# Optimization experiments

Measured on AMD Instinct MI355X. Metric: run time of the kernel, lower is better.

## Reference

```python
import jax, jax.numpy as jnp
import numpy as np

B, N, FIN, HID, HEADS, LAYERS = 2048, 62, 128, 512, 8, 3
FOUT = HID // HEADS  # 64


def setup_inputs() -> dict:
    key = jax.random.key(0)
    ks = jax.random.split(key, 12)
    x = jax.random.normal(ks[0], (B, N, FIN), dtype=jnp.float32)
    adj = jax.random.randint(ks[1], (B, N, N), 0, 2, dtype=jnp.int32)
    # BatchNorm1d(62) params (eval mode, running stats)
    bn_gamma = jax.random.normal(ks[2], (N,), dtype=jnp.float32) * 0.1 + 1.0
    bn_beta = jax.random.normal(ks[3], (N,), dtype=jnp.float32) * 0.1
    bn_mean = jax.random.normal(ks[4], (N,), dtype=jnp.float32) * 0.1
    bn_var = jax.random.uniform(ks[5], (N,), dtype=jnp.float32, minval=0.5, maxval=1.5)
    # input MLP
    W_mlp = jax.random.normal(ks[6], (FIN, HID), dtype=jnp.float32) / np.sqrt(FIN)
    b_mlp = jnp.zeros((HID,), dtype=jnp.float32)
    # GAT params: one W [HID, FOUT] and one a [2*FOUT] per (layer, head)
    W_gat = jax.random.normal(ks[7], (LAYERS, HEADS, HID, FOUT), dtype=jnp.float32) / np.sqrt(HID)
    a_gat = jax.random.normal(ks[8], (LAYERS, HEADS, 2 * FOUT), dtype=jnp.float32) / np.sqrt(2 * FOUT)
    # output head
    W_out = jax.random.normal(ks[9], (HID, 3), dtype=jnp.float32) / np.sqrt(HID)
    b_out = jnp.zeros((3,), dtype=jnp.float32)
    return {
        "x": x, "adj": adj,
        "bn_gamma": bn_gamma, "bn_beta": bn_beta, "bn_mean": bn_mean, "bn_var": bn_var,
        "W_mlp": W_mlp, "b_mlp": b_mlp,
        "W_gat": W_gat, "a_gat": a_gat,
        "W_out": W_out, "b_out": b_out,
    }


def reference(x, adj, bn_gamma, bn_beta, bn_mean, bn_var, W_mlp, b_mlp, W_gat, a_gat, W_out, b_out):
    eps = 1e-5
    alpha = 0.2  # LeakyReLU slope
    # BatchNorm1d over the node dim (C=62), eval mode
    xb = (x - bn_mean[None, :, None]) * (bn_gamma / jnp.sqrt(bn_var + eps))[None, :, None] + bn_beta[None, :, None]
    h_x = xb @ W_mlp + b_mlp  # [B, N, HID]
    mask = adj > 0  # [B, N, N]
    n_layers, n_heads, _, f_out = W_gat.shape
    for l in range(n_layers):
        # all heads at once: h [H, B, N, FOUT]
        h = jnp.einsum('bnf,hfd->hbnd', h_x, W_gat[l])
        a1 = a_gat[l][:, :f_out]   # multiplies the repeat(1,N,1) part -> h_j
        a2 = a_gat[l][:, f_out:]   # multiplies the repeat(1,1,N) part -> h_i
        f1 = jnp.einsum('hbnd,hd->hbn', h, a1)  # per-node source term
        f2 = jnp.einsum('hbnd,hd->hbn', h, a2)  # per-node dest term
        # e[h,b,i,j] = leaky(a2.h_i + a1.h_j)  (matches cat/repeat layout)
        e = jax.nn.leaky_relu(f2[:, :, :, None] + f1[:, :, None, :], alpha)
        e = jnp.where(mask[None], e, jnp.float32(-9e15))
        # torch F.softmax(attention, dim=1) on [B,N,N] -> axis=2 here (the i axis)
        att = jax.nn.softmax(e, axis=2)
        hp = jnp.einsum('hbij,hbjd->hbid', att, h)
        hp = jax.nn.elu(hp)
        # concat heads on feature dim -> [B, N, HID]
        h_x = jnp.transpose(hp, (1, 2, 0, 3)).reshape(h_x.shape[0], h_x.shape[1], n_heads * f_out)
    pooled = jnp.sum(h_x, axis=1)  # [B, HID]
    logits = pooled @ W_out + b_out  # [B, 3]
    return jax.nn.log_softmax(logits, axis=-1)
```

## Files before the change

kernel.cpp:

```cpp
#include <hip/hip_runtime.h>
#include <cstdint>
#include <cstddef>

#define B_ 2048
#define N_ 62
#define FIN_ 128
#define HID_ 512
#define HEADS_ 8
#define FOUT_ 64
#define LAYERS_ 3
#define M_ (B_*N_)

typedef __bf16 bf16x8 __attribute__((ext_vector_type(8)));
typedef float  f32x4  __attribute__((ext_vector_type(4)));
typedef unsigned short u16;

static __device__ __forceinline__ u16 f2bf(float f) {
    union { float f; uint32_t u; } v; v.f = f;
    uint32_t u = v.u;
    return (u16)((u + 0x7fffu + ((u >> 16) & 1u)) >> 16);
}
static __device__ __forceinline__ float bf2f(u16 s) {
    union { uint32_t u; float f; } v; v.u = ((uint32_t)s) << 16;
    return v.f;
}
static __device__ __forceinline__ float rdlane(float v, int l) {
    union { float f; int i; } a, b; a.f = v;
    b.i = __builtin_amdgcn_readlane(a.i, l);
    return b.f;
}

__global__ __launch_bounds__(256) void repack_w(
    const float* __restrict__ Wm, const float* __restrict__ Wg,
    u16* __restrict__ wmlp_t, u16* __restrict__ wgat_t)
{
    int idx = blockIdx.x * 256 + threadIdx.x;
    const int T1 = HID_ * FIN_;
    const int T2 = LAYERS_ * HID_ * HID_;
    if (idx < T1) {
        int n = idx / FIN_, k = idx % FIN_;
        wmlp_t[idx] = f2bf(Wm[k * HID_ + n]);
    } else if (idx < T1 + T2) {
        int j = idx - T1;
        int l = j / (HID_ * HID_);
        int r = j % (HID_ * HID_);
        int n = r / HID_, k = r % HID_;
        wgat_t[j] = f2bf(Wg[(((size_t)(l * HEADS_ + (n >> 6))) * HID_ + k) * FOUT_ + (n & 63)]);
    }
}

__global__ __launch_bounds__(256) void build_masks(
    const int* __restrict__ adj, uint64_t* __restrict__ masks,
    uint64_t* __restrict__ masksT)
{
    __shared__ uint32_t m32[128];
    const int b = blockIdx.x, tid = threadIdx.x;
    if (tid < 128) m32[tid] = 0;
    __syncthreads();
    const int* a = adj + (size_t)b * N_ * N_;
    for (int idx = tid; idx < N_ * N_; idx += 256) {
        int i = idx / N_, j = idx % N_;
        if (a[idx] > 0) atomicOr(&m32[i * 2 + (j >> 5)], 1u << (j & 31));
    }
    __syncthreads();
    if (tid < 128) ((uint32_t*)(masks + (size_t)b * 64))[tid] = m32[tid];
    if (tid < 64) {
        int j = tid;
        uint64_t c = 0;
        for (int i = 0; i < N_; i++) {
            uint64_t bit = (m32[i * 2 + (j >> 5)] >> (j & 31)) & 1u;
            c |= bit << i;
        }
        masksT[(size_t)b * 64 + j] = c;
    }
}

#define S_IN 520
#define S_T  72
#define S_X  136
#define X0   28160

__global__ __launch_bounds__(512, 4) void gat_fused(
    const float* __restrict__ x,
    const float* __restrict__ bng, const float* __restrict__ bnb,
    const float* __restrict__ bnm, const float* __restrict__ bnv,
    const u16* __restrict__ wmlp_t, const float* __restrict__ bm,
    const u16* __restrict__ wgat_t, const float* __restrict__ ag,
    const uint64_t* __restrict__ masks, const uint64_t* __restrict__ masksT,
    const float* __restrict__ Wout, const float* __restrict__ bout,
    float* __restrict__ out)
{
    __shared__ __align__(16) u16 buf[36864];
    __shared__ uint64_t msk[64];
    __shared__ __align__(16) float fstat[1032];
    float* F1 = fstat;
    float* LS = fstat + 512;

    const int tid = threadIdx.x, b = blockIdx.x;
    const int wave = tid >> 6, lane = tid & 63;
    const int lr = lane & 15, lq = lane >> 4;
    const int w64 = wave * 64;

    const uint64_t cm = masksT[(size_t)b * 64 + lane];
    const uint32_t cml = (uint32_t)cm, cmh = (uint32_t)(cm >> 32);

    {
        const float* xg = x + (size_t)b * N_ * FIN_;
        for (int idx = tid; idx < 2048; idx += 512) {
            int n = idx >> 5, kq = idx & 31;
            ushort4 o = {0, 0, 0, 0};
            if (n < N_) {
                float s = bng[n] * rsqrtf(bnv[n] + 1e-5f);
                float sh = bnb[n] - bnm[n] * s;
                float4 v = *(const float4*)(xg + n * FIN_ + kq * 4);
                o.x = f2bf(v.x * s + sh); o.y = f2bf(v.y * s + sh);
                o.z = f2bf(v.z * s + sh); o.w = f2bf(v.w * s + sh);
            }
            *(ushort4*)&buf[X0 + n * S_X + kq * 4] = o;
        }
        if (tid < 64) msk[tid] = (tid < N_) ? masks[(size_t)b * 64 + tid] : 0ull;
    }
    __syncthreads();

    {
        f32x4 acc[4][4];
#pragma unroll
        for (int mt = 0; mt < 4; mt++)
#pragma unroll
            for (int nt = 0; nt < 4; nt++) acc[mt][nt] = (f32x4){0.f, 0.f, 0.f, 0.f};
        const int c0 = w64;
#pragma unroll
        for (int kt = 0; kt < 4; kt++) {
            int k0 = kt * 32;
            bf16x8 af[4];
#pragma unroll
            for (int mt = 0; mt < 4; mt++)
                af[mt] = *(const bf16x8*)&buf[X0 + (mt * 16 + lr) * S_X + k0 + lq * 8];
#pragma unroll
            for (int nt = 0; nt < 4; nt++) {
                bf16x8 bfr = *(const bf16x8*)(wmlp_t + (size_t)(c0 + nt * 16 + lr) * FIN_ + k0 + lq * 8);
#pragma unroll
                for (int mt = 0; mt < 4; mt++)
                    acc[mt][nt] = __builtin_amdgcn_mfma_f32_16x16x32_bf16(
                        af[mt], bfr, acc[mt][nt], 0, 0, 0);
            }
        }
        __syncthreads();
        float bl[4];
#pragma unroll
        for (int nt = 0; nt < 4; nt++) bl[nt] = bm[c0 + nt * 16 + lr];
#pragma unroll
        for (int mt = 0; mt < 4; mt++)
#pragma unroll
            for (int nt = 0; nt < 4; nt++)
#pragma unroll
                for (int r = 0; r < 4; r++) {
                    int row = mt * 16 + lq * 4 + r;
                    buf[row * S_IN + c0 + nt * 16 + lr] =
                        (row < N_) ? f2bf(acc[mt][nt][r] + bl[nt]) : (u16)0;
                }
    }
    __syncthreads();

#pragma unroll 1
    for (int l = 0; l < LAYERS_; l++) {
        const u16* wp = wgat_t + ((size_t)l * HID_ + w64) * HID_;
        const float* a1 = ag + (size_t)l * HEADS_ * 2 * FOUT_ + wave * 128;

        f32x4 acc[4][4];
#pragma unroll
        for (int mt = 0; mt < 4; mt++)
#pragma unroll
            for (int nt = 0; nt < 4; nt++) acc[mt][nt] = (f32x4){0.f, 0.f, 0.f, 0.f};
#pragma unroll 4
        for (int kt = 0; kt < 16; kt++) {
            int k0 = kt * 32;
            bf16x8 af[4];
#pragma unroll
            for (int mt = 0; mt < 4; mt++)
                af[mt] = *(const bf16x8*)&buf[(mt * 16 + lr) * S_IN + k0 + lq * 8];
#pragma unroll
            for (int nt = 0; nt < 4; nt++) {
                bf16x8 bfr = *(const bf16x8*)(wp + (size_t)(nt * 16 + lr) * HID_ + k0 + lq * 8);
#pragma unroll
                for (int mt = 0; mt < 4; mt++)
                    acc[mt][nt] = __builtin_amdgcn_mfma_f32_16x16x32_bf16(
                        af[mt], bfr, acc[mt][nt], 0, 0, 0);
            }
        }
        __syncthreads();

#pragma unroll
        for (int mt = 0; mt < 4; mt++)
#pragma unroll
            for (int nt = 0; nt < 4; nt++) {
                ushort4 pk;
                pk.x = f2bf(acc[mt][nt][0]); pk.y = f2bf(acc[mt][nt][1]);
                pk.z = f2bf(acc[mt][nt][2]); pk.w = f2bf(acc[mt][nt][3]);
                *(ushort4*)&buf[(w64 + nt * 16 + lr) * S_T + mt * 16 + lq * 4] = pk;
            }

        float p1 = 0.f, p2 = 0.f;
#pragma unroll 8
        for (int d = 0; d < 64; d++) {
            float hv = bf2f(buf[(w64 + d) * S_T + lane]);
            p1 = fmaf(hv, a1[d], p1);
            p2 = fmaf(hv, a1[64 + d], p2);
        }

        float M = -3.0e38f;
#pragma unroll
        for (int i = 0; i < N_; i++) {
            float f2i = rdlane(p2, i);
            uint32_t bit = ((i < 32 ? cml : cmh) >> (i & 31)) & 1u;
            M = fmaxf(M, bit ? f2i : -3.0e38f);
        }
        float vm = M + p1;
        float m = fmaxf(fmaxf(vm, 0.2f * vm), -9e15f);
        float ssum = 0.f;
#pragma unroll
        for (int i = 0; i < N_; i++) {
            float f2i = rdlane(p2, i);
            float v = f2i + p1;
            v = fmaxf(v, 0.2f * v);
            uint32_t bit = ((i < 32 ? cml : cmh) >> (i & 31)) & 1u;
            float e = bit ? v : -9e15f;
            ssum += __expf(e - m);
        }
        F1[w64 + lane] = p1;
        LS[w64 + lane] = m + __logf(ssum);

        f32x4 acc2[4][4];
#pragma unroll
        for (int mt = 0; mt < 4; mt++)
#pragma unroll
            for (int nt = 0; nt < 4; nt++) acc2[mt][nt] = (f32x4){0.f, 0.f, 0.f, 0.f};
        float f2r[4];
#pragma unroll
        for (int mt = 0; mt < 4; mt++) f2r[mt] = __shfl(p2, mt * 16 + lr, 64);
#pragma unroll
        for (int kt = 0; kt < 2; kt++) {
            int j0 = kt * 32 + lq * 8;
            f32x4 f1a = *(const f32x4*)&F1[w64 + j0];
            f32x4 f1b = *(const f32x4*)&F1[w64 + j0 + 4];
            f32x4 la  = *(const f32x4*)&LS[w64 + j0];
            f32x4 lb  = *(const f32x4*)&LS[w64 + j0 + 4];
            bf16x8 hb[4];
#pragma unroll
            for (int nt = 0; nt < 4; nt++)
                hb[nt] = *(const bf16x8*)&buf[(w64 + nt * 16 + lr) * S_T + kt * 32 + lq * 8];
#pragma unroll
            for (int mt = 0; mt < 4; mt++) {
                uint64_t mi = msk[mt * 16 + lr];
                uint32_t sh = (uint32_t)(mi >> (kt * 32)) >> (lq * 8);
                bf16x8 pf;
#pragma unroll
                for (int t = 0; t < 8; t++) {
                    float f1t = t < 4 ? f1a[t] : f1b[t - 4];
                    float lst = t < 4 ? la[t]  : lb[t - 4];
                    float v = f2r[mt] + f1t;
                    v = fmaxf(v, 0.2f * v);
                    float e = ((sh >> t) & 1u) ? v : -9e15f;
                    pf[t] = (__bf16)__expf(e - lst);
                }
#pragma unroll
                for (int nt = 0; nt < 4; nt++)
                    acc2[mt][nt] = __builtin_amdgcn_mfma_f32_16x16x32_bf16(
                        pf, hb[nt], acc2[mt][nt], 0, 0, 0);
            }
        }
        __syncthreads();

#pragma unroll
        for (int mt = 0; mt < 4; mt++)
#pragma unroll
            for (int nt = 0; nt < 4; nt++)
#pragma unroll
                for (int r = 0; r < 4; r++) {
                    float v = acc2[mt][nt][r];
                    v = v > 0.f ? v : __expf(v) - 1.f;
                    int row = mt * 16 + lq * 4 + r;
                    buf[row * S_IN + w64 + nt * 16 + lr] =
                        (row < N_) ? f2bf(v) : (u16)0;
                }
        __syncthreads();
    }

    {
        float s = 0.f;
#pragma unroll 2
        for (int n = 0; n < N_; n++) s += bf2f(buf[n * S_IN + tid]);
        fstat[tid] = s;
    }
    __syncthreads();
    if (tid < 192) {
        int c = tid >> 6, ln = tid & 63;
        float p = 0.f;
#pragma unroll
        for (int k = ln; k < HID_; k += 64) p += fstat[k] * Wout[k * 3 + c];
        for (int off = 32; off > 0; off >>= 1) p += __shfl_down(p, off, 64);
        if (ln == 0) fstat[1024 + c] = p + bout[c];
    }
    __syncthreads();
    if (tid == 0) {
        float l0 = fstat[1024], l1 = fstat[1025], l2 = fstat[1026];
        float mm = fmaxf(l0, fmaxf(l1, l2));
        float s = __expf(l0 - mm) + __expf(l1 - mm) + __expf(l2 - mm);
        float ls = mm + logf(s);
        out[b * 3 + 0] = l0 - ls;
        out[b * 3 + 1] = l1 - ls;
        out[b * 3 + 2] = l2 - ls;
    }
}

extern "C" void kernel_launch(void* const* d_in, const int* in_sizes, int n_in,
                              void* d_out, int out_size, void* d_ws, size_t ws_size,
                              hipStream_t stream)
{
    const float* x   = (const float*)d_in[0];
    const int*   adj = (const int*)d_in[1];
    const float* bng = (const float*)d_in[2];
    const float* bnb = (const float*)d_in[3];
    const float* bnm = (const float*)d_in[4];
    const float* bnv = (const float*)d_in[5];
    const float* Wm  = (const float*)d_in[6];
    const float* bm  = (const float*)d_in[7];
    const float* Wg  = (const float*)d_in[8];
    const float* ag  = (const float*)d_in[9];
    const float* Wo  = (const float*)d_in[10];
    const float* bo  = (const float*)d_in[11];
    float* out = (float*)d_out;

    uint64_t* masks  = (uint64_t*)d_ws;
    uint64_t* masksT = masks + (size_t)B_ * 64;
    u16* wmlp_t = (u16*)(masksT + (size_t)B_ * 64);
    u16* wgat_t = wmlp_t + (size_t)HID_ * FIN_;

    int rep_total = HID_ * FIN_ + LAYERS_ * HID_ * HID_;
    repack_w<<<(rep_total + 255) / 256, 256, 0, stream>>>(Wm, Wg, wmlp_t, wgat_t);
    build_masks<<<B_, 256, 0, stream>>>(adj, masks, masksT);

    gat_fused<<<B_, 512, 0, stream>>>(
        x, bng, bnb, bnm, bnv, wmlp_t, bm, wgat_t, ag,
        masks, masksT, Wo, bo, out);
}
```

Baseline: 698.8 us.

## Fold attention vectors into GAT weights and simplify softmax statistics

Precomputes W·a1 and W·a2 (scaled by log2e) as two extra output columns of each head's weight matrix, so the attention logits come out of the projection MFMA instead of a separate 64-step dot-product loop. The softmax max now uses an unmasked upper bound via a wave reduction instead of a masked 62-step scan, and exponentials use exp2. The MLP and aggregation MFMAs are transposed so results are written as packed 4-element stores. In exchange, each head does a fifth N-tile of MFMA work (80 columns, 16 of them padding), the logits are rounded to bf16 weights, and the unmasked max can underflow sums, which is guarded by a clamp.

Result: slower. 996.5 us (+42.6%).

```diff
diff --git a/kernel.cpp b/kernel.cpp
--- a/kernel.cpp
+++ b/kernel.cpp
@@ -15,6 +15,19 @@
 typedef float  f32x4  __attribute__((ext_vector_type(4)));
 typedef unsigned short u16;
 
+#define LOG2E 1.4426950408889634f
+
+#if __has_builtin(__builtin_amdgcn_exp2f)
+#define EXP2F(x) __builtin_amdgcn_exp2f(x)
+#else
+#define EXP2F(x) exp2f(x)
+#endif
+#if __has_builtin(__builtin_amdgcn_logf)
+#define LOG2F(x) __builtin_amdgcn_logf(x)
+#else
+#define LOG2F(x) log2f(x)
+#endif
+
 static __device__ __forceinline__ u16 f2bf(float f) {
     union { float f; uint32_t u; } v; v.f = f;
     uint32_t u = v.u;
@@ -32,20 +45,33 @@
 
 __global__ __launch_bounds__(256) void repack_w(
     const float* __restrict__ Wm, const float* __restrict__ Wg,
-    u16* __restrict__ wmlp_t, u16* __restrict__ wgat_t)
+    const float* __restrict__ ag,
+    u16* __restrict__ wmlp_t, u16* __restrict__ wgat2)
 {
     int idx = blockIdx.x * 256 + threadIdx.x;
     const int T1 = HID_ * FIN_;
-    const int T2 = LAYERS_ * HID_ * HID_;
+    const int T2 = LAYERS_ * HEADS_ * 80 * HID_;
     if (idx < T1) {
         int n = idx / FIN_, k = idx % FIN_;
         wmlp_t[idx] = f2bf(Wm[k * HID_ + n]);
     } else if (idx < T1 + T2) {
         int j = idx - T1;
-        int l = j / (HID_ * HID_);
-        int r = j % (HID_ * HID_);
+        int lh = j / (80 * HID_);
+        int r  = j % (80 * HID_);
         int n = r / HID_, k = r % HID_;
-        wgat_t[j] = f2bf(Wg[(((size_t)(l * HEADS_ + (n >> 6))) * HID_ + k) * FOUT_ + (n & 63)]);
+        float v;
+        if (n < 64) {
+            v = Wg[((size_t)lh * HID_ + k) * FOUT_ + n];
+        } else if (n < 66) {
+            const float* ap = ag + (size_t)lh * 128 + (n - 64) * 64;
+            const float* wrow = Wg + ((size_t)lh * HID_ + k) * FOUT_;
+            float s = 0.f;
+            for (int d = 0; d < 64; d++) s += wrow[d] * ap[d];
+            v = s * LOG2E;
+        } else {
+            v = 0.f;
+        }
+        wgat2[j] = f2bf(v);
     }
 }
 
@@ -85,16 +111,17 @@
     const float* __restrict__ bng, const float* __restrict__ bnb,
     const float* __restrict__ bnm, const float* __restrict__ bnv,
     const u16* __restrict__ wmlp_t, const float* __restrict__ bm,
-    const u16* __restrict__ wgat_t, const float* __restrict__ ag,
+    const u16* __restrict__ wgat2,
     const uint64_t* __restrict__ masks, const uint64_t* __restrict__ masksT,
     const float* __restrict__ Wout, const float* __restrict__ bout,
     float* __restrict__ out)
 {
     __shared__ __align__(16) u16 buf[36864];
     __shared__ uint64_t msk[64];
-    __shared__ __align__(16) float fstat[1032];
+    __shared__ __align__(16) float fstat[1544];
     float* F1 = fstat;
-    float* LS = fstat + 512;
+    float* F2 = fstat + 512;
+    float* LS = fstat + 1024;
 
     const int tid = threadIdx.x, b = blockIdx.x;
     const int wave = tid >> 6, lane = tid & 63;
@@ -122,6 +149,10 @@
     }
     __syncthreads();
 
+    uint64_t mi4[4];
+#pragma unroll
+    for (int it = 0; it < 4; it++) mi4[it] = msk[it * 16 + lr];
+
     {
         f32x4 acc[4][4];
 #pragma unroll
@@ -132,46 +163,54 @@
 #pragma unroll
         for (int kt = 0; kt < 4; kt++) {
             int k0 = kt * 32;
-            bf16x8 af[4];
-#pragma unroll
-            for (int mt = 0; mt < 4; mt++)
-                af[mt] = *(const bf16x8*)&buf[X0 + (mt * 16 + lr) * S_X + k0 + lq * 8];
+            bf16x8 wf[4], xf[4];
+#pragma unroll
+            for (int mt = 0; mt < 4; mt++)
+                wf[mt] = *(const bf16x8*)(wmlp_t + (size_t)(c0 + mt * 16 + lr) * FIN_ + k0 + lq * 8);
+#pragma unroll
+            for (int nt = 0; nt < 4; nt++)
+                xf[nt] = *(const bf16x8*)&buf[X0 + (nt * 16 + lr) * S_X + k0 + lq * 8];
+#pragma unroll
+            for (int mt = 0; mt < 4; mt++)
+#pragma unroll
+                for (int nt = 0; nt < 4; nt++)
+                    acc[mt][nt] = __builtin_amdgcn_mfma_f32_16x16x32_bf16(
+                        wf[mt], xf[nt], acc[mt][nt], 0, 0, 0);
+        }
+        __syncthreads();
+        f32x4 bl[4];
+#pragma unroll
+        for (int mt = 0; mt < 4; mt++)
+            bl[mt] = *(const f32x4*)&bm[c0 + mt * 16 + lq * 4];
+#pragma unroll
+        for (int mt = 0; mt < 4; mt++)
 #pragma unroll
             for (int nt = 0; nt < 4; nt++) {
-                bf16x8 bfr = *(const bf16x8*)(wmlp_t + (size_t)(c0 + nt * 16 + lr) * FIN_ + k0 + lq * 8);
-#pragma unroll
-                for (int mt = 0; mt < 4; mt++)
-                    acc[mt][nt] = __builtin_amdgcn_mfma_f32_16x16x32_bf16(
-                        af[mt], bfr, acc[mt][nt], 0, 0, 0);
-            }
-        }
-        __syncthreads();
-        float bl[4];
-#pragma unroll
-        for (int nt = 0; nt < 4; nt++) bl[nt] = bm[c0 + nt * 16 + lr];
-#pragma unroll
-        for (int mt = 0; mt < 4; mt++)
-#pragma unroll
-            for (int nt = 0; nt < 4; nt++)
-#pragma unroll
-                for (int r = 0; r < 4; r++) {
-                    int row = mt * 16 + lq * 4 + r;
-                    buf[row * S_IN + c0 + nt * 16 + lr] =
-                        (row < N_) ? f2bf(acc[mt][nt][r] + bl[nt]) : (u16)0;
-                }
+                int node = nt * 16 + lr;
+                ushort4 pk;
+                pk.x = f2bf(acc[mt][nt][0] + bl[mt][0]);
+                pk.y = f2bf(acc[mt][nt][1] + bl[mt][1]);
+                pk.z = f2bf(acc[mt][nt][2] + bl[mt][2]);
+                pk.w = f2bf(acc[mt][nt][3] + bl[mt][3]);
+                if (node < N_)
+                    *(ushort4*)&buf[node * S_IN + c0 + mt * 16 + lq * 4] = pk;
+            }
+        if (lane < 16) {
+            uint4 z = {0u, 0u, 0u, 0u};
+            *(uint4*)&buf[(N_ + (lane >> 3)) * S_IN + c0 + (lane & 7) * 8] = z;
+        }
     }
     __syncthreads();
 
 #pragma unroll 1
     for (int l = 0; l < LAYERS_; l++) {
-        const u16* wp = wgat_t + ((size_t)l * HID_ + w64) * HID_;
-        const float* a1 = ag + (size_t)l * HEADS_ * 2 * FOUT_ + wave * 128;
-
-        f32x4 acc[4][4];
-#pragma unroll
-        for (int mt = 0; mt < 4; mt++)
-#pragma unroll
-            for (int nt = 0; nt < 4; nt++) acc[mt][nt] = (f32x4){0.f, 0.f, 0.f, 0.f};
+        const u16* wp = wgat2 + (size_t)(l * HEADS_ + wave) * 80 * HID_;
+
+        f32x4 acc[4][5];
+#pragma unroll
+        for (int mt = 0; mt < 4; mt++)
+#pragma unroll
+            for (int nt = 0; nt < 5; nt++) acc[mt][nt] = (f32x4){0.f, 0.f, 0.f, 0.f};
 #pragma unroll 4
         for (int kt = 0; kt < 16; kt++) {
             int k0 = kt * 32;
@@ -180,7 +219,7 @@
             for (int mt = 0; mt < 4; mt++)
                 af[mt] = *(const bf16x8*)&buf[(mt * 16 + lr) * S_IN + k0 + lq * 8];
 #pragma unroll
-            for (int nt = 0; nt < 4; nt++) {
+            for (int nt = 0; nt < 5; nt++) {
                 bf16x8 bfr = *(const bf16x8*)(wp + (size_t)(nt * 16 + lr) * HID_ + k0 + lq * 8);
 #pragma unroll
                 for (int mt = 0; mt < 4; mt++)
@@ -188,6 +227,36 @@
                         af[mt], bfr, acc[mt][nt], 0, 0, 0);
             }
         }
+
+        if (lr < 2) {
+            float* Fp = lr ? F2 : F1;
+#pragma unroll
+            for (int mt = 0; mt < 4; mt++)
+#pragma unroll
+                for (int r = 0; r < 4; r++)
+                    Fp[w64 + mt * 16 + lq * 4 + r] = acc[mt][4][r];
+        }
+        float p1 = F1[w64 + lane];
+        float p2 = F2[w64 + lane];
+        float pm = (lane < N_) ? p2 : -3.0e38f;
+#pragma unroll
+        for (int off = 32; off; off >>= 1) pm = fmaxf(pm, __shfl_xor(pm, off, 64));
+        float vm = pm + p1;
+        float m = fmaxf(vm, 0.2f * vm);
+        float s0 = 0.f, s1 = 0.f;
+#pragma unroll
+        for (int i = 0; i < N_; i += 2) {
+            float fa = rdlane(p2, i), fb = rdlane(p2, i + 1);
+            float va = fa + p1, vb = fb + p1;
+            va = fmaxf(va, 0.2f * va); vb = fmaxf(vb, 0.2f * vb);
+            float ea = EXP2F(va - m), eb = EXP2F(vb - m);
+            uint32_t w = (i < 32) ? cml : cmh;
+            s0 += ((w >> (i & 31)) & 1u) ? ea : 0.f;
+            s1 += ((w >> ((i + 1) & 31)) & 1u) ? eb : 0.f;
+        }
+        float ssum = fmaxf(s0 + s1, 1e-35f);
+        LS[w64 + lane] = m + LOG2F(ssum);
+
         __syncthreads();
 
 #pragma unroll
@@ -200,44 +269,14 @@
                 *(ushort4*)&buf[(w64 + nt * 16 + lr) * S_T + mt * 16 + lq * 4] = pk;
             }
 
-        float p1 = 0.f, p2 = 0.f;
-#pragma unroll 8
-        for (int d = 0; d < 64; d++) {
-            float hv = bf2f(buf[(w64 + d) * S_T + lane]);
-            p1 = fmaf(hv, a1[d], p1);
-            p2 = fmaf(hv, a1[64 + d], p2);
-        }
-
-        float M = -3.0e38f;
-#pragma unroll
-        for (int i = 0; i < N_; i++) {
-            float f2i = rdlane(p2, i);
-            uint32_t bit = ((i < 32 ? cml : cmh) >> (i & 31)) & 1u;
-            M = fmaxf(M, bit ? f2i : -3.0e38f);
-        }
-        float vm = M + p1;
-        float m = fmaxf(fmaxf(vm, 0.2f * vm), -9e15f);
-        float ssum = 0.f;
-#pragma unroll
-        for (int i = 0; i < N_; i++) {
-            float f2i = rdlane(p2, i);
-            float v = f2i + p1;
-            v = fmaxf(v, 0.2f * v);
-            uint32_t bit = ((i < 32 ? cml : cmh) >> (i & 31)) & 1u;
-            float e = bit ? v : -9e15f;
-            ssum += __expf(e - m);
-        }
-        F1[w64 + lane] = p1;
-        LS[w64 + lane] = m + __logf(ssum);
-
         f32x4 acc2[4][4];
 #pragma unroll
         for (int mt = 0; mt < 4; mt++)
 #pragma unroll
-            for (int nt = 0; nt < 4; nt++) acc2[mt][nt] = (f32x4){0.f, 0.f, 0.f, 0.f};
-        float f2r[4];
-#pragma unroll
-        for (int mt = 0; mt < 4; mt++) f2r[mt] = __shfl(p2, mt * 16 + lr, 64);
+            for (int it = 0; it < 4; it++) acc2[mt][it] = (f32x4){0.f, 0.f, 0.f, 0.f};
+        float f2v[4];
+#pragma unroll
+        for (int it = 0; it < 4; it++) f2v[it] = F2[w64 + it * 16 + lr];
 #pragma unroll
         for (int kt = 0; kt < 2; kt++) {
             int j0 = kt * 32 + lq * 8;
@@ -245,28 +284,28 @@
             f32x4 f1b = *(const f32x4*)&F1[w64 + j0 + 4];
             f32x4 la  = *(const f32x4*)&LS[w64 + j0];
             f32x4 lb  = *(const f32x4*)&LS[w64 + j0 + 4];
-            bf16x8 hb[4];
-#pragma unroll
-            for (int nt = 0; nt < 4; nt++)
-                hb[nt] = *(const bf16x8*)&buf[(w64 + nt * 16 + lr) * S_T + kt * 32 + lq * 8];
-#pragma unroll
-            for (int mt = 0; mt < 4; mt++) {
-                uint64_t mi = msk[mt * 16 + lr];
-                uint32_t sh = (uint32_t)(mi >> (kt * 32)) >> (lq * 8);
+            bf16x8 ha[4];
+#pragma unroll
+            for (int mt = 0; mt < 4; mt++)
+                ha[mt] = *(const bf16x8*)&buf[(w64 + mt * 16 + lr) * S_T + kt * 32 + lq * 8];
+#pragma unroll
+            for (int it = 0; it < 4; it++) {
+                uint32_t sh = (uint32_t)(mi4[it] >> (kt * 32)) >> (lq * 8);
                 bf16x8 pf;
 #pragma unroll
                 for (int t = 0; t < 8; t++) {
                     float f1t = t < 4 ? f1a[t] : f1b[t - 4];
                     float lst = t < 4 ? la[t]  : lb[t - 4];
-                    float v = f2r[mt] + f1t;
+                    float v = f2v[it] + f1t;
                     v = fmaxf(v, 0.2f * v);
-                    float e = ((sh >> t) & 1u) ? v : -9e15f;
-                    pf[t] = (__bf16)__expf(e - lst);
+                    float p = EXP2F(v - lst);
+                    p = ((sh >> t) & 1u) ? p : 0.f;
+                    pf[t] = (__bf16)p;
                 }
 #pragma unroll
-                for (int nt = 0; nt < 4; nt++)
-                    acc2[mt][nt] = __builtin_amdgcn_mfma_f32_16x16x32_bf16(
-                        pf, hb[nt], acc2[mt][nt], 0, 0, 0);
+                for (int mt = 0; mt < 4; mt++)
+                    acc2[mt][it] = __builtin_amdgcn_mfma_f32_16x16x32_bf16(
+                        ha[mt], pf, acc2[mt][it], 0, 0, 0);
             }
         }
         __syncthreads();
@@ -274,15 +313,22 @@
 #pragma unroll
         for (int mt = 0; mt < 4; mt++)
 #pragma unroll
-            for (int nt = 0; nt < 4; nt++)
+            for (int it = 0; it < 4; it++) {
+                int i = it * 16 + lr;
+                ushort4 pk;
 #pragma unroll
                 for (int r = 0; r < 4; r++) {
-                    float v = acc2[mt][nt][r];
+                    float v = acc2[mt][it][r];
                     v = v > 0.f ? v : __expf(v) - 1.f;
-                    int row = mt * 16 + lq * 4 + r;
-                    buf[row * S_IN + w64 + nt * 16 + lr] =
-                        (row < N_) ? f2bf(v) : (u16)0;
+                    ((u16*)&pk)[r] = f2bf(v);
                 }
+                if (i < N_)
+                    *(ushort4*)&buf[i * S_IN + w64 + mt * 16 + lq * 4] = pk;
+            }
+        if (lane < 16) {
+            uint4 z = {0u, 0u, 0u, 0u};
+            *(uint4*)&buf[(N_ + (lane >> 3)) * S_IN + w64 + (lane & 7) * 8] = z;
+        }
         __syncthreads();
     }
 
@@ -299,11 +345,11 @@
 #pragma unroll
         for (int k = ln; k < HID_; k += 64) p += fstat[k] * Wout[k * 3 + c];
         for (int off = 32; off > 0; off >>= 1) p += __shfl_down(p, off, 64);
-        if (ln == 0) fstat[1024 + c] = p + bout[c];
+        if (ln == 0) fstat[1536 + c] = p + bout[c];
     }
     __syncthreads();
     if (tid == 0) {
-        float l0 = fstat[1024], l1 = fstat[1025], l2 = fstat[1026];
+        float l0 = fstat[1536], l1 = fstat[1537], l2 = fstat[1538];
         float mm = fmaxf(l0, fmaxf(l1, l2));
         float s = __expf(l0 - mm) + __expf(l1 - mm) + __expf(l2 - mm);
         float ls = mm + logf(s);
@@ -334,13 +380,13 @@
     uint64_t* masks  = (uint64_t*)d_ws;
     uint64_t* masksT = masks + (size_t)B_ * 64;
     u16* wmlp_t = (u16*)(masksT + (size_t)B_ * 64);
-    u16* wgat_t = wmlp_t + (size_t)HID_ * FIN_;
-
-    int rep_total = HID_ * FIN_ + LAYERS_ * HID_ * HID_;
-    repack_w<<<(rep_total + 255) / 256, 256, 0, stream>>>(Wm, Wg, wmlp_t, wgat_t);
+    u16* wgat2  = wmlp_t + (size_t)HID_ * FIN_;
+
+    int rep_total = HID_ * FIN_ + LAYERS_ * HEADS_ * 80 * HID_;
+    repack_w<<<(rep_total + 255) / 256, 256, 0, stream>>>(Wm, Wg, ag, wmlp_t, wgat2);
     build_masks<<<B_, 256, 0, stream>>>(adj, masks, masksT);
 
     gat_fused<<<B_, 512, 0, stream>>>(
-        x, bng, bnb, bnm, bnv, wmlp_t, bm, wgat_t, ag,
+        x, bng, bnb, bnm, bnv, wmlp_t, bm, wgat2,
         masks, masksT, Wo, bo, out);
 }
```
